# Optimization experiments

Hardware: AMD Instinct MI355X
Metric: run time of the kernel (lower is better)

## Reference

```python
import jax, jax.numpy as jnp
import numpy as np

GROUPS = 4
EPS = 1e-5


def _distill(x, fc1_w, fc1_b, ln_w, ln_b, fc2_w, fc2_b):
    # x: [N, cs, H, W] -> gated x (the 'input * gate' output of ChannelGate_sub)
    p = x.mean(axis=(2, 3))                     # global avg pool -> [N, cs]
    p = p @ fc1_w.T + fc1_b                     # 1x1 conv == dense on pooled vec
    mu = p.mean(axis=-1, keepdims=True)         # LayerNorm over [cs,1,1] == over channel dim
    var = jnp.mean((p - mu) ** 2, axis=-1, keepdims=True)
    p = (p - mu) * jax.lax.rsqrt(var + EPS) * ln_w + ln_b
    p = jax.nn.relu(p)
    p = p @ fc2_w.T + fc2_b
    g = jax.nn.sigmoid(p)                       # [N, cs]
    return x * g[:, :, None, None]


def _forward(x, cweight, cbias, sweight, sbias, gn_w, gn_b,
             fc1_w, fc1_b, ln_w, ln_b, fc2_w, fc2_b):
    b, c, h, w = x.shape
    x = x.reshape(b * GROUPS, c // GROUPS, h, w)
    cs = c // (2 * GROUPS)
    x0, x1 = x[:, :cs], x[:, cs:]               # chunk(2, dim=1)

    # channel-attention branch
    xn = x0.mean(axis=(2, 3), keepdims=True)    # [N, cs, 1, 1]
    xn = cweight * xn + cbias
    xn = x0 * jax.nn.sigmoid(xn)
    x_reid_0 = x0 - xn
    xn = xn + _distill(x_reid_0, fc1_w, fc1_b, ln_w, ln_b, fc2_w, fc2_b)

    # spatial-attention branch: GroupNorm(cs groups, cs channels) == per-channel instance norm
    mu = x1.mean(axis=(2, 3), keepdims=True)
    var = jnp.mean((x1 - mu) ** 2, axis=(2, 3), keepdims=True)
    xs = (x1 - mu) * jax.lax.rsqrt(var + EPS)
    xs = xs * gn_w[None, :, None, None] + gn_b[None, :, None, None]
    xs = sweight * xs + sbias
    xs = x1 * jax.nn.sigmoid(xs)
    x_reid_1 = x1 - xs
    xs = xs + _distill(x_reid_1, fc1_w, fc1_b, ln_w, ln_b, fc2_w, fc2_b)

    out = jnp.concatenate([xn, xs], axis=1)
    return out.reshape(b, c, h, w)


def setup_inputs() -> dict:
    key = jax.random.key(0)
    ks = jax.random.split(key, 14)
    B, C, H, W = 32, 256, 64, 64
    cs = C // (2 * GROUPS)  # 32
    s = 0.1
    return {
        "x": jax.random.normal(ks[0], (B, C, H, W), jnp.float32),
        "cweight": jax.random.normal(ks[1], (1, cs, 1, 1), jnp.float32) * s,
        "cbias": jnp.ones((1, cs, 1, 1), jnp.float32) + jax.random.normal(ks[2], (1, cs, 1, 1), jnp.float32) * s,
        "sweight": jax.random.normal(ks[3], (1, cs, H, W), jnp.float32) * s,
        "sbias": jnp.ones((1, cs, 1, 1), jnp.float32) + jax.random.normal(ks[4], (1, cs, 1, 1), jnp.float32) * s,
        "gn_w": jnp.ones((cs,), jnp.float32) + jax.random.normal(ks[5], (cs,), jnp.float32) * s,
        "gn_b": jax.random.normal(ks[6], (cs,), jnp.float32) * s,
        "fc1_w": jax.random.normal(ks[7], (cs, cs), jnp.float32) * (1.0 / np.sqrt(cs)),
        "fc1_b": jax.random.normal(ks[8], (cs,), jnp.float32) * s,
        "ln_w": jnp.ones((cs,), jnp.float32) + jax.random.normal(ks[9], (cs,), jnp.float32) * s,
        "ln_b": jax.random.normal(ks[10], (cs,), jnp.float32) * s,
        "fc2_w": jax.random.normal(ks[11], (cs, cs), jnp.float32) * (1.0 / np.sqrt(cs)),
        "fc2_b": jax.random.normal(ks[12], (cs,), jnp.float32) * s,
    }


def reference(x, cweight, cbias, sweight, sbias, gn_w, gn_b,
              fc1_w, fc1_b, ln_w, ln_b, fc2_w, fc2_b):
    return _forward(x, cweight, cbias, sweight, sbias, gn_w, gn_b,
                    fc1_w, fc1_b, ln_w, ln_b, fc2_w, fc2_b)
```

## Files before the change

kernel.cpp:

```cpp
#include <hip/hip_runtime.h>
#include <math.h>

#define HW 4096
#define CS 32
#define NS 128
#define NPLANES 8192
#define EPS 1e-5f

typedef float vfloat4 __attribute__((ext_vector_type(4)));

__device__ __forceinline__ float sigmoidf_(float x) {
    return 1.0f / (1.0f + __expf(-x));
}

__device__ __forceinline__ void nt_store4(float4* p, float4 v) {
    __builtin_nontemporal_store(*(const vfloat4*)&v, (vfloat4*)p);
}

__device__ __forceinline__ float block_reduce(float s, float* ls, int tid) {
    for (int off = 32; off > 0; off >>= 1) s += __shfl_down(s, off, 64);
    const int wave = tid >> 6, lane = tid & 63;
    if (lane == 0) ls[wave] = s;
    __syncthreads();
    return ls[0] + ls[1] + ls[2] + ls[3];
}

__global__ __launch_bounds__(256) void pass1_kernel(
    const float* __restrict__ x,
    const float* __restrict__ gnw, const float* __restrict__ gnb,
    const float* __restrict__ sw,  const float* __restrict__ sb,
    float* __restrict__ sums0, float* __restrict__ mu1,
    float* __restrict__ rs1,   float* __restrict__ sumxs) {
    const int P = blockIdx.x;
    const int n = P >> 6, cc = P & 63;
    const int tid = threadIdx.x;
    const float4* xp = (const float4*)(x + (size_t)P * HW);
    __shared__ float ls[4];
    __shared__ float bc[2];

    if (cc < CS) {
        float s = 0.f;
#pragma unroll
        for (int k = 0; k < 4; ++k) {
            float4 v = xp[tid + k * 256];
            s += v.x + v.y + v.z + v.w;
        }
        s = block_reduce(s, ls, tid);
        if (tid == 0) sums0[n * CS + cc] = s;
    } else {
        const int c = cc - CS;
        float4 v[4];
        float s = 0.f, s2 = 0.f;
#pragma unroll
        for (int k = 0; k < 4; ++k) {
            v[k] = xp[tid + k * 256];
            s  += v[k].x + v[k].y + v[k].z + v[k].w;
            s2 += v[k].x * v[k].x + v[k].y * v[k].y
                + v[k].z * v[k].z + v[k].w * v[k].w;
        }
        for (int off = 32; off > 0; off >>= 1) {
            s  += __shfl_down(s, off, 64);
            s2 += __shfl_down(s2, off, 64);
        }
        __shared__ float ls2[4];
        const int wave = tid >> 6, lane = tid & 63;
        if (lane == 0) { ls[wave] = s; ls2[wave] = s2; }
        __syncthreads();
        if (tid == 0) {
            float st  = ls[0] + ls[1] + ls[2] + ls[3];
            float s2t = ls2[0] + ls2[1] + ls2[2] + ls2[3];
            float mu  = st * (1.0f / HW);
            float var = s2t * (1.0f / HW) - mu * mu;
            float rs  = rsqrtf(var + EPS);
            mu1[n * CS + c] = mu;
            rs1[n * CS + c] = rs;
            bc[0] = mu; bc[1] = rs;
        }
        __syncthreads();
        const float mu = bc[0], rs = bc[1];
        const float a  = gnw[c] * rs;
        const float b0 = gnb[c] - mu * a;
        const float sbv = sb[c];
        const float4* wp = (const float4*)(sw + (size_t)c * HW);
        float sx = 0.f;
#pragma unroll
        for (int k = 0; k < 4; ++k) {
            float4 w = wp[tid + k * 256];
            sx += v[k].x * sigmoidf_(w.x * (v[k].x * a + b0) + sbv);
            sx += v[k].y * sigmoidf_(w.y * (v[k].y * a + b0) + sbv);
            sx += v[k].z * sigmoidf_(w.z * (v[k].z * a + b0) + sbv);
            sx += v[k].w * sigmoidf_(w.w * (v[k].w * a + b0) + sbv);
        }
        __syncthreads();
        sx = block_reduce(sx, ls, tid);
        if (tid == 0) sumxs[n * CS + c] = sx;
    }
}

__global__ __launch_bounds__(256) void out_kernel(
    const float* __restrict__ x, float* __restrict__ out,
    const float* __restrict__ sums0,
    const float* __restrict__ mu1, const float* __restrict__ rs1,
    const float* __restrict__ sumxs,
    const float* __restrict__ cw,  const float* __restrict__ cb,
    const float* __restrict__ gnw, const float* __restrict__ gnb,
    const float* __restrict__ sw,  const float* __restrict__ sb,
    const float* __restrict__ fc1w, const float* __restrict__ fc1b,
    const float* __restrict__ lnw, const float* __restrict__ lnb,
    const float* __restrict__ fc2w, const float* __restrict__ fc2b) {
    const int P = blockIdx.x;
    const int n = P >> 6, cc = P & 63;
    const int tid = threadIdx.x;
    const int branch = (cc >= CS);
    const int c0 = cc & 31;

    __shared__ float pS[CS], qS[CS], rS[CS], g0S[CS];
    __shared__ float scaleS;

    if (tid < CS) {
        float pv;
        if (!branch) {
            float mean = sums0[n * CS + tid] * (1.0f / HW);
            float g0 = sigmoidf_(cw[tid] * mean + cb[tid]);
            g0S[tid] = g0;
            pv = mean * (1.0f - g0);
        } else {
            pv = mu1[n * CS + tid] - sumxs[n * CS + tid] * (1.0f / HW);
        }
        pS[tid] = pv;
    }
    __syncthreads();
    if (tid < CS) {
        float qv = fc1b[tid];
        for (int j = 0; j < CS; ++j) qv += fc1w[tid * CS + j] * pS[j];
        qS[tid] = qv;
    }
    __syncthreads();
    if (tid < CS) {
        float mu = 0.f;
        for (int j = 0; j < CS; ++j) mu += qS[j];
        mu *= (1.0f / CS);
        float var = 0.f;
        for (int j = 0; j < CS; ++j) { float d = qS[j] - mu; var += d * d; }
        var *= (1.0f / CS);
        float qn = (qS[tid] - mu) * rsqrtf(var + EPS) * lnw[tid] + lnb[tid];
        rS[tid] = fmaxf(qn, 0.f);
    }
    __syncthreads();
    if (tid < 64) {
        float t = (tid < CS) ? fc2w[c0 * CS + tid] * rS[tid] : 0.f;
        for (int off = 32; off > 0; off >>= 1) t += __shfl_down(t, off, 64);
        if (tid == 0) {
            float gd = sigmoidf_(t + fc2b[c0]);
            scaleS = branch ? gd : (g0S[c0] + (1.0f - g0S[c0]) * gd);
        }
    }
    __syncthreads();

    const float4* xp = (const float4*)(x + (size_t)P * HW);
    float4* op = (float4*)(out + (size_t)P * HW);

    if (!branch) {
        const float scale = scaleS;
#pragma unroll
        for (int k = 0; k < 4; ++k) {
            float4 v = xp[tid + k * 256];
            v.x *= scale; v.y *= scale; v.z *= scale; v.w *= scale;
            nt_store4(op + tid + k * 256, v);
        }
    } else {
        const float g  = scaleS;
        const float mu = mu1[n * CS + c0], rs = rs1[n * CS + c0];
        const float a  = gnw[c0] * rs;
        const float b0 = gnb[c0] - mu * a;
        const float sbv = sb[c0];
        const float4* wp = (const float4*)(sw + (size_t)c0 * HW);
#pragma unroll
        for (int k = 0; k < 4; ++k) {
            float4 v = xp[tid + k * 256];
            float4 w = wp[tid + k * 256];
            float4 o; float sg;
            sg = sigmoidf_(w.x * (v.x * a + b0) + sbv); o.x = v.x * (sg + (1.f - sg) * g);
            sg = sigmoidf_(w.y * (v.y * a + b0) + sbv); o.y = v.y * (sg + (1.f - sg) * g);
            sg = sigmoidf_(w.z * (v.z * a + b0) + sbv); o.z = v.z * (sg + (1.f - sg) * g);
            sg = sigmoidf_(w.w * (v.w * a + b0) + sbv); o.w = v.w * (sg + (1.f - sg) * g);
            nt_store4(op + tid + k * 256, o);
        }
    }
}

extern "C" void kernel_launch(void* const* d_in, const int* in_sizes, int n_in,
                              void* d_out, int out_size, void* d_ws, size_t ws_size,
                              hipStream_t stream) {
    const float* x    = (const float*)d_in[0];
    const float* cw   = (const float*)d_in[1];
    const float* cb   = (const float*)d_in[2];
    const float* sw   = (const float*)d_in[3];
    const float* sb   = (const float*)d_in[4];
    const float* gnw  = (const float*)d_in[5];
    const float* gnb  = (const float*)d_in[6];
    const float* fc1w = (const float*)d_in[7];
    const float* fc1b = (const float*)d_in[8];
    const float* lnw  = (const float*)d_in[9];
    const float* lnb  = (const float*)d_in[10];
    const float* fc2w = (const float*)d_in[11];
    const float* fc2b = (const float*)d_in[12];
    float* out = (float*)d_out;
    float* ws  = (float*)d_ws;

    float* sums0 = ws;
    float* mu1   = ws + 4096;
    float* rs1   = ws + 8192;
    float* sumxs = ws + 12288;

    pass1_kernel<<<NPLANES, 256, 0, stream>>>(x, gnw, gnb, sw, sb,
                                              sums0, mu1, rs1, sumxs);
    out_kernel<<<NPLANES, 256, 0, stream>>>(x, out, sums0, mu1, rs1, sumxs,
                                            cw, cb, gnw, gnb, sw, sb,
                                            fc1w, fc1b, lnw, lnb, fc2w, fc2b);
}
```

Baseline: 67.77 us.

## Fuse stats and output passes into one kernel per sample-branch

Replaces the two 8192-block kernels with a single kernel launched as 256 blocks of 1024 threads, one block per (sample, branch) pair covering all 32 channel planes. Each 32-lane slice reduces one plane, and the tiny MLP gate is computed in-block with shuffles instead of through a global workspace. This removes a launch and the workspace round trip, and it re-reads x within the block, where it may still be in cache. The cost is that only 256 large blocks are in flight, which may underfill the GPU, and the branch-1 blocks read x three times with sigmoid work done twice.

```diff
diff --git a/kernel.cpp b/kernel.cpp
--- a/kernel.cpp
+++ b/kernel.cpp
@@ -4,7 +4,6 @@
 #define HW 4096
 #define CS 32
 #define NS 128
-#define NPLANES 8192
 #define EPS 1e-5f
 
 typedef float vfloat4 __attribute__((ext_vector_type(4)));
@@ -17,174 +16,126 @@
     __builtin_nontemporal_store(*(const vfloat4*)&v, (vfloat4*)p);
 }
 
-__device__ __forceinline__ float block_reduce(float s, float* ls, int tid) {
-    for (int off = 32; off > 0; off >>= 1) s += __shfl_down(s, off, 64);
-    const int wave = tid >> 6, lane = tid & 63;
-    if (lane == 0) ls[wave] = s;
-    __syncthreads();
-    return ls[0] + ls[1] + ls[2] + ls[3];
-}
-
-__global__ __launch_bounds__(256) void pass1_kernel(
-    const float* __restrict__ x,
+__global__ __launch_bounds__(1024, 1) void fused_kernel(
+    const float* __restrict__ x, float* __restrict__ out,
+    const float* __restrict__ cw,  const float* __restrict__ cb,
+    const float* __restrict__ sw,  const float* __restrict__ sb,
     const float* __restrict__ gnw, const float* __restrict__ gnb,
-    const float* __restrict__ sw,  const float* __restrict__ sb,
-    float* __restrict__ sums0, float* __restrict__ mu1,
-    float* __restrict__ rs1,   float* __restrict__ sumxs) {
-    const int P = blockIdx.x;
-    const int n = P >> 6, cc = P & 63;
-    const int tid = threadIdx.x;
-    const float4* xp = (const float4*)(x + (size_t)P * HW);
-    __shared__ float ls[4];
-    __shared__ float bc[2];
-
-    if (cc < CS) {
-        float s = 0.f;
-#pragma unroll
-        for (int k = 0; k < 4; ++k) {
-            float4 v = xp[tid + k * 256];
-            s += v.x + v.y + v.z + v.w;
-        }
-        s = block_reduce(s, ls, tid);
-        if (tid == 0) sums0[n * CS + cc] = s;
-    } else {
-        const int c = cc - CS;
-        float4 v[4];
-        float s = 0.f, s2 = 0.f;
-#pragma unroll
-        for (int k = 0; k < 4; ++k) {
-            v[k] = xp[tid + k * 256];
-            s  += v[k].x + v[k].y + v[k].z + v[k].w;
-            s2 += v[k].x * v[k].x + v[k].y * v[k].y
-                + v[k].z * v[k].z + v[k].w * v[k].w;
-        }
-        for (int off = 32; off > 0; off >>= 1) {
-            s  += __shfl_down(s, off, 64);
-            s2 += __shfl_down(s2, off, 64);
-        }
-        __shared__ float ls2[4];
-        const int wave = tid >> 6, lane = tid & 63;
-        if (lane == 0) { ls[wave] = s; ls2[wave] = s2; }
-        __syncthreads();
-        if (tid == 0) {
-            float st  = ls[0] + ls[1] + ls[2] + ls[3];
-            float s2t = ls2[0] + ls2[1] + ls2[2] + ls2[3];
-            float mu  = st * (1.0f / HW);
-            float var = s2t * (1.0f / HW) - mu * mu;
-            float rs  = rsqrtf(var + EPS);
-            mu1[n * CS + c] = mu;
-            rs1[n * CS + c] = rs;
-            bc[0] = mu; bc[1] = rs;
-        }
-        __syncthreads();
-        const float mu = bc[0], rs = bc[1];
-        const float a  = gnw[c] * rs;
-        const float b0 = gnb[c] - mu * a;
-        const float sbv = sb[c];
-        const float4* wp = (const float4*)(sw + (size_t)c * HW);
-        float sx = 0.f;
-#pragma unroll
-        for (int k = 0; k < 4; ++k) {
-            float4 w = wp[tid + k * 256];
-            sx += v[k].x * sigmoidf_(w.x * (v[k].x * a + b0) + sbv);
-            sx += v[k].y * sigmoidf_(w.y * (v[k].y * a + b0) + sbv);
-            sx += v[k].z * sigmoidf_(w.z * (v[k].z * a + b0) + sbv);
-            sx += v[k].w * sigmoidf_(w.w * (v[k].w * a + b0) + sbv);
-        }
-        __syncthreads();
-        sx = block_reduce(sx, ls, tid);
-        if (tid == 0) sumxs[n * CS + c] = sx;
-    }
-}
-
-__global__ __launch_bounds__(256) void out_kernel(
-    const float* __restrict__ x, float* __restrict__ out,
-    const float* __restrict__ sums0,
-    const float* __restrict__ mu1, const float* __restrict__ rs1,
-    const float* __restrict__ sumxs,
-    const float* __restrict__ cw,  const float* __restrict__ cb,
-    const float* __restrict__ gnw, const float* __restrict__ gnb,
-    const float* __restrict__ sw,  const float* __restrict__ sb,
     const float* __restrict__ fc1w, const float* __restrict__ fc1b,
     const float* __restrict__ lnw, const float* __restrict__ lnb,
     const float* __restrict__ fc2w, const float* __restrict__ fc2b) {
-    const int P = blockIdx.x;
-    const int n = P >> 6, cc = P & 63;
+    const int blk = blockIdx.x;
+    const int n = blk >> 1, branch = blk & 1;
     const int tid = threadIdx.x;
-    const int branch = (cc >= CS);
-    const int c0 = cc & 31;
+    const int p  = tid >> 5;
+    const int sl = tid & 31;
 
-    __shared__ float pS[CS], qS[CS], rS[CS], g0S[CS];
-    __shared__ float scaleS;
+    __shared__ float muS[CS], rsS[CS], pvS[CS], g0S[CS], scS[CS];
 
-    if (tid < CS) {
-        float pv;
-        if (!branch) {
-            float mean = sums0[n * CS + tid] * (1.0f / HW);
-            float g0 = sigmoidf_(cw[tid] * mean + cb[tid]);
-            g0S[tid] = g0;
-            pv = mean * (1.0f - g0);
-        } else {
-            pv = mu1[n * CS + tid] - sumxs[n * CS + tid] * (1.0f / HW);
+    const size_t base4 = ((size_t)(n * 64 + branch * CS)) * 1024;
+    const float4* xp = (const float4*)x + base4 + (size_t)p * 1024;
+    float4*       op = (float4*)out    + base4 + (size_t)p * 1024;
+
+    if (!branch) {
+        float s = 0.f;
+#pragma unroll 8
+        for (int k = 0; k < 32; ++k) {
+            float4 v = xp[k * 32 + sl];
+            s += v.x + v.y + v.z + v.w;
         }
-        pS[tid] = pv;
-    }
-    __syncthreads();
-    if (tid < CS) {
-        float qv = fc1b[tid];
-        for (int j = 0; j < CS; ++j) qv += fc1w[tid * CS + j] * pS[j];
-        qS[tid] = qv;
-    }
-    __syncthreads();
-    if (tid < CS) {
-        float mu = 0.f;
-        for (int j = 0; j < CS; ++j) mu += qS[j];
-        mu *= (1.0f / CS);
-        float var = 0.f;
-        for (int j = 0; j < CS; ++j) { float d = qS[j] - mu; var += d * d; }
-        var *= (1.0f / CS);
-        float qn = (qS[tid] - mu) * rsqrtf(var + EPS) * lnw[tid] + lnb[tid];
-        rS[tid] = fmaxf(qn, 0.f);
-    }
-    __syncthreads();
-    if (tid < 64) {
-        float t = (tid < CS) ? fc2w[c0 * CS + tid] * rS[tid] : 0.f;
-        for (int off = 32; off > 0; off >>= 1) t += __shfl_down(t, off, 64);
-        if (tid == 0) {
-            float gd = sigmoidf_(t + fc2b[c0]);
-            scaleS = branch ? gd : (g0S[c0] + (1.0f - g0S[c0]) * gd);
+        for (int off = 16; off; off >>= 1) s += __shfl_down(s, off, 64);
+        if (sl == 0) {
+            float mean = s * (1.0f / HW);
+            float g0 = sigmoidf_(cw[p] * mean + cb[p]);
+            g0S[p] = g0;
+            pvS[p] = mean * (1.0f - g0);
+        }
+    } else {
+        float s = 0.f, s2 = 0.f;
+#pragma unroll 8
+        for (int k = 0; k < 32; ++k) {
+            float4 v = xp[k * 32 + sl];
+            s  += v.x + v.y + v.z + v.w;
+            s2 += v.x * v.x + v.y * v.y + v.z * v.z + v.w * v.w;
+        }
+        for (int off = 16; off; off >>= 1) {
+            s  += __shfl_down(s,  off, 64);
+            s2 += __shfl_down(s2, off, 64);
+        }
+        if (sl == 0) {
+            float mu  = s * (1.0f / HW);
+            float var = s2 * (1.0f / HW) - mu * mu;
+            muS[p] = mu;
+            rsS[p] = rsqrtf(var + EPS);
         }
     }
     __syncthreads();
 
-    const float4* xp = (const float4*)(x + (size_t)P * HW);
-    float4* op = (float4*)(out + (size_t)P * HW);
+    if (branch) {
+        const float mu = muS[p], rs = rsS[p];
+        const float a   = gnw[p] * rs;
+        const float b0  = gnb[p] - mu * a;
+        const float sbv = sb[p];
+        const float4* wp = (const float4*)sw + (size_t)p * 1024;
+        float sx = 0.f;
+#pragma unroll 4
+        for (int k = 0; k < 32; ++k) {
+            float4 v = xp[k * 32 + sl];
+            float4 w = wp[k * 32 + sl];
+            sx += v.x * sigmoidf_(w.x * (v.x * a + b0) + sbv);
+            sx += v.y * sigmoidf_(w.y * (v.y * a + b0) + sbv);
+            sx += v.z * sigmoidf_(w.z * (v.z * a + b0) + sbv);
+            sx += v.w * sigmoidf_(w.w * (v.w * a + b0) + sbv);
+        }
+        for (int off = 16; off; off >>= 1) sx += __shfl_down(sx, off, 64);
+        if (sl == 0) pvS[p] = mu - sx * (1.0f / HW);
+    }
+    __syncthreads();
 
+    if (tid < CS) {
+        const int c = tid;
+        float qv = fc1b[c];
+        for (int j = 0; j < CS; ++j) qv += fc1w[c * CS + j] * pvS[j];
+        float bs = qv, bs2 = qv * qv;
+        for (int m = 1; m < 32; m <<= 1) {
+            bs  += __shfl_xor(bs,  m, 64);
+            bs2 += __shfl_xor(bs2, m, 64);
+        }
+        float mu  = bs * (1.0f / CS);
+        float var = bs2 * (1.0f / CS) - mu * mu;
+        float qn  = (qv - mu) * rsqrtf(var + EPS) * lnw[c] + lnb[c];
+        float r   = fmaxf(qn, 0.f);
+        float sv  = fc2b[c];
+        for (int j = 0; j < CS; ++j) sv += fc2w[c * CS + j] * __shfl(r, j, 64);
+        float gd = sigmoidf_(sv);
+        scS[c] = branch ? gd : (g0S[c] + (1.0f - g0S[c]) * gd);
+    }
+    __syncthreads();
+
+    const float sc = scS[p];
     if (!branch) {
-        const float scale = scaleS;
-#pragma unroll
-        for (int k = 0; k < 4; ++k) {
-            float4 v = xp[tid + k * 256];
-            v.x *= scale; v.y *= scale; v.z *= scale; v.w *= scale;
-            nt_store4(op + tid + k * 256, v);
+#pragma unroll 8
+        for (int k = 0; k < 32; ++k) {
+            float4 v = xp[k * 32 + sl];
+            v.x *= sc; v.y *= sc; v.z *= sc; v.w *= sc;
+            nt_store4(op + k * 32 + sl, v);
         }
     } else {
-        const float g  = scaleS;
-        const float mu = mu1[n * CS + c0], rs = rs1[n * CS + c0];
-        const float a  = gnw[c0] * rs;
-        const float b0 = gnb[c0] - mu * a;
-        const float sbv = sb[c0];
-        const float4* wp = (const float4*)(sw + (size_t)c0 * HW);
-#pragma unroll
-        for (int k = 0; k < 4; ++k) {
-            float4 v = xp[tid + k * 256];
-            float4 w = wp[tid + k * 256];
+        const float mu = muS[p], rs = rsS[p];
+        const float a   = gnw[p] * rs;
+        const float b0  = gnb[p] - mu * a;
+        const float sbv = sb[p];
+        const float4* wp = (const float4*)sw + (size_t)p * 1024;
+#pragma unroll 4
+        for (int k = 0; k < 32; ++k) {
+            float4 v = xp[k * 32 + sl];
+            float4 w = wp[k * 32 + sl];
             float4 o; float sg;
-            sg = sigmoidf_(w.x * (v.x * a + b0) + sbv); o.x = v.x * (sg + (1.f - sg) * g);
-            sg = sigmoidf_(w.y * (v.y * a + b0) + sbv); o.y = v.y * (sg + (1.f - sg) * g);
-            sg = sigmoidf_(w.z * (v.z * a + b0) + sbv); o.z = v.z * (sg + (1.f - sg) * g);
-            sg = sigmoidf_(w.w * (v.w * a + b0) + sbv); o.w = v.w * (sg + (1.f - sg) * g);
-            nt_store4(op + tid + k * 256, o);
+            sg = sigmoidf_(w.x * (v.x * a + b0) + sbv); o.x = v.x * (sg + (1.f - sg) * sc);
+            sg = sigmoidf_(w.y * (v.y * a + b0) + sbv); o.y = v.y * (sg + (1.f - sg) * sc);
+            sg = sigmoidf_(w.z * (v.z * a + b0) + sbv); o.z = v.z * (sg + (1.f - sg) * sc);
+            sg = sigmoidf_(w.w * (v.w * a + b0) + sbv); o.w = v.w * (sg + (1.f - sg) * sc);
+            nt_store4(op + k * 32 + sl, o);
         }
     }
 }
@@ -206,16 +157,8 @@
     const float* fc2w = (const float*)d_in[11];
     const float* fc2b = (const float*)d_in[12];
     float* out = (float*)d_out;
-    float* ws  = (float*)d_ws;
 
-    float* sums0 = ws;
-    float* mu1   = ws + 4096;
-    float* rs1   = ws + 8192;
-    float* sumxs = ws + 12288;
-
-    pass1_kernel<<<NPLANES, 256, 0, stream>>>(x, gnw, gnb, sw, sb,
-                                              sums0, mu1, rs1, sumxs);
-    out_kernel<<<NPLANES, 256, 0, stream>>>(x, out, sums0, mu1, rs1, sumxs,
-                                            cw, cb, gnw, gnb, sw, sb,
-                                            fc1w, fc1b, lnw, lnb, fc2w, fc2b);
+    fused_kernel<<<NS * 2, 1024, 0, stream>>>(x, out, cw, cb, sw, sb,
+                                              gnw, gnb, fc1w, fc1b,
+                                              lnw, lnb, fc2w, fc2b);
 }
```

New measurement: 85.33 us. +25.9%, slower.
